# Optimization experiments

Measured on AMD Instinct MI355X. Metric: run time of the kernel, lower is better.

The kernel has to match this reference:

```python
import jax, jax.numpy as jnp
import numpy as np

N_HEADS = 32
N_KV = 8
GROUPS = 4
D_HEAD = 64
ROPE_BASE = 10000.0


def _rope_tables(seq_len):
    # inv_freq over even dims, emb = [freqs, freqs] along last axis (torch cat([outer]*2))
    inv_freq = 1.0 / (ROPE_BASE ** (jnp.arange(0, D_HEAD, 2, dtype=jnp.float32) / D_HEAD))
    t = jnp.arange(seq_len, dtype=jnp.float32)
    freqs = jnp.outer(t, inv_freq)                      # [S, D_HEAD/2]
    emb = jnp.concatenate([freqs, freqs], axis=-1)      # [S, D_HEAD]
    return jnp.cos(emb), jnp.sin(emb)


def _rotate_half(x):
    h = x.shape[-1] // 2
    return jnp.concatenate([-x[..., h:], x[..., :h]], axis=-1)


def setup_inputs() -> dict:
    key = jax.random.key(0)
    ks = jax.random.split(key, 5)
    B, S, D = 4, 2048, 2048
    s = 0.02
    return {
        "x": jax.random.normal(ks[0], (B, S, D), dtype=jnp.float32),
        "Wq": jax.random.normal(ks[1], (D, D), dtype=jnp.float32) * s,
        "Wk": jax.random.normal(ks[2], (N_KV * D_HEAD, D), dtype=jnp.float32) * s,
        "Wv": jax.random.normal(ks[3], (N_KV * D_HEAD, D), dtype=jnp.float32) * s,
        "Wo": jax.random.normal(ks[4], (D, D), dtype=jnp.float32) * s,
        "temperature": jnp.float32(1.0),
    }


def reference(x, Wq, Wk, Wv, Wo, temperature):
    B, S, D = x.shape
    # QKV projections (torch Linear: x @ W.T)
    Q = jnp.einsum('bsd,ed->bse', x, Wq).reshape(B, S, N_HEADS, D_HEAD).transpose(0, 2, 1, 3)
    K = jnp.einsum('bsd,ed->bse', x, Wk).reshape(B, S, N_KV, D_HEAD).transpose(0, 2, 1, 3)
    V = jnp.einsum('bsd,ed->bse', x, Wv).reshape(B, S, N_KV, D_HEAD).transpose(0, 2, 1, 3)

    # RoPE (offset=0, no past_kv)
    cos, sin = _rope_tables(S)          # [S, D_HEAD]
    cos = cos[None, None]
    sin = sin[None, None]
    Q = Q * cos + _rotate_half(Q) * sin
    K = K * cos + _rotate_half(K) * sin

    kv_cache = (K, V)  # pre-expansion cache, as in original

    # GQA expand: each kv head repeated GROUPS times along head axis
    Ke = jnp.repeat(K, GROUPS, axis=1)  # [B, N_HEADS, S, D_HEAD]
    Ve = jnp.repeat(V, GROUPS, axis=1)

    # scale uses .item() in torch -> constant w.r.t. autograd
    scale = (D_HEAD ** -0.5) / jnp.maximum(jnp.abs(temperature), 1e-6)
    scale = jax.lax.stop_gradient(scale)

    scores = jnp.einsum('bhqd,bhkd->bhqk', Q, Ke) * scale
    causal = jnp.tril(jnp.ones((S, S), dtype=bool))
    scores = jnp.where(causal[None, None], scores, jnp.finfo(scores.dtype).min)
    attn = jax.nn.softmax(scores, axis=-1)
    out = jnp.einsum('bhqk,bhkd->bhqd', attn, Ve)       # [B, H, S, D_HEAD]

    out = out.transpose(0, 2, 1, 3).reshape(B, S, D)
    y = jnp.einsum('bsd,ed->bse', out, Wo)
    return (y, kv_cache[0], kv_cache[1])
```

## Files before the change

### kernel.cpp

```cpp
#include <hip/hip_runtime.h>

#define S_LEN  2048
#define DMODEL 2048
#define NH     32
#define NKV    8
#define DH     64

typedef _Float16 h8   __attribute__((ext_vector_type(8)));
typedef _Float16 h4   __attribute__((ext_vector_type(4)));
typedef float    f32x4 __attribute__((ext_vector_type(4)));

__device__ __forceinline__ void load_lds16(const _Float16* g, _Float16* l) {
  typedef const __attribute__((address_space(1))) unsigned int* gp_t;
  typedef __attribute__((address_space(3))) unsigned int* lp_t;
  __builtin_amdgcn_global_load_lds((gp_t)g, (lp_t)l, 16, 0, 0);
}

#define N8_X  2097152
#define N8_WQ 524288
#define N8_WK 131072
#define N8_WV 131072
#define N8_WO 524288
#define N8_ALL (N8_X + N8_WQ + N8_WK + N8_WV + N8_WO)
__global__ void cvt_all(const float* __restrict__ x, const float* __restrict__ wq,
                        const float* __restrict__ wk, const float* __restrict__ wv,
                        const float* __restrict__ wo, _Float16* __restrict__ dst) {
  int stride = gridDim.x * blockDim.x;
  for (int i = blockIdx.x * blockDim.x + threadIdx.x; i < N8_ALL; i += stride) {
    const float* s;
    int off;
    if (i < N8_X) { s = x; off = i; }
    else if (i < N8_X + N8_WQ) { s = wq; off = i - N8_X; }
    else if (i < N8_X + N8_WQ + N8_WK) { s = wk; off = i - (N8_X + N8_WQ); }
    else if (i < N8_X + N8_WQ + N8_WK + N8_WV) { s = wv; off = i - (N8_X + N8_WQ + N8_WK); }
    else { s = wo; off = i - (N8_X + N8_WQ + N8_WK + N8_WV); }
    float4 a = ((const float4*)s)[2 * off];
    float4 b = ((const float4*)s)[2 * off + 1];
    h8 v = {(_Float16)a.x, (_Float16)a.y, (_Float16)a.z, (_Float16)a.w,
            (_Float16)b.x, (_Float16)b.y, (_Float16)b.z, (_Float16)b.w};
    ((h8*)dst)[i] = v;
  }
}

__global__ void rope_table_k(float2* __restrict__ tab) {
  int i = blockIdx.x * blockDim.x + threadIdx.x;
  int s = i >> 5, d = i & 31;
  float invf = (float)exp2(-(double)d * 0.4152410118609203);
  float angf = (float)s * invf;
  double a = (double)angf;
  const double twopi = 6.283185307179586476925287;
  a -= floor(a / twopi) * twopi;
  tab[i] = make_float2((float)cos(a), (float)sin(a));
}

template <int MODE>
__global__ __launch_bounds__(512, 2) void gemm256(
    const _Float16* __restrict__ A, const _Float16* __restrict__ Bm,
    _Float16* __restrict__ qH, _Float16* __restrict__ kH, float* __restrict__ kF,
    _Float16* __restrict__ vH, float* __restrict__ vF, float* __restrict__ yF,
    const float2* __restrict__ rtab, const float* __restrict__ tptr) {
  __shared__ __align__(16) _Float16 lA[2][256 * 64];
  __shared__ __align__(16) _Float16 lB[2][128 * 64];
  const int Kd = 2048;
  int t = threadIdx.x;
  int w = t >> 6, lane = t & 63;
  int n0 = blockIdx.x * 128, m0 = blockIdx.y * 256;
  int wr = w >> 1, wc = w & 1;
  int lq = lane & 15, hi = lane >> 4;

  int swz = ((lane & 7) ^ (lane >> 3)) * 8;
  const _Float16* pA = A + (size_t)(m0 + w * 32 + (lane >> 3)) * Kd + swz;
  const _Float16* pB = Bm + (size_t)(n0 + w * 16 + (lane >> 3)) * Kd + swz;
  int dA = (w * 32) * 64;
  int dB = (w * 16) * 64;

  f32x4 z4 = {0.f, 0.f, 0.f, 0.f};
  f32x4 acc[4][4];
#pragma unroll
  for (int i = 0; i < 4; i++)
#pragma unroll
    for (int j = 0; j < 4; j++) acc[i][j] = z4;

#pragma unroll
  for (int i = 0; i < 2; i++)
    load_lds16(pB + (size_t)(i * 8) * Kd, &lB[0][dB + i * 8 * 64]);
#pragma unroll
  for (int i = 0; i < 4; i++)
    load_lds16(pA + (size_t)(i * 8) * Kd, &lA[0][dA + i * 8 * 64]);

  const int NT = Kd / 64;
  for (int tt = 0; tt < NT; tt++) {
    int cur = tt & 1, nxt = cur ^ 1;

    asm volatile("s_waitcnt vmcnt(4)" ::: "memory");
    __builtin_amdgcn_s_barrier();

    if (tt + 1 < NT) {
      int k0n = (tt + 1) * 64;
#pragma unroll
      for (int i = 0; i < 2; i++)
        load_lds16(pB + (size_t)(i * 8) * Kd + k0n, &lB[nxt][dB + i * 8 * 64]);
#pragma unroll
      for (int i = 0; i < 4; i++)
        load_lds16(pA + (size_t)(i * 8) * Kd + k0n, &lA[nxt][dA + i * 8 * 64]);
    }

    h8 bf[4][2];
#pragma unroll
    for (int j = 0; j < 4; j++)
#pragma unroll
      for (int s = 0; s < 2; s++)
        bf[j][s] = *(const h8*)&lB[cur][(wc * 64 + j * 16 + lq) * 64 + (((s * 4 + hi) ^ (lq & 7)) * 8)];

    if (tt + 1 < NT) {
      asm volatile("s_waitcnt vmcnt(6)" ::: "memory");
    } else {
      asm volatile("s_waitcnt vmcnt(0)" ::: "memory");
    }
    __builtin_amdgcn_s_barrier();

#pragma unroll
    for (int p = 0; p < 4; p++) {
      h8 af[2];
#pragma unroll
      for (int s = 0; s < 2; s++)
        af[s] = *(const h8*)&lA[cur][(wr * 64 + p * 16 + lq) * 64 + (((s * 4 + hi) ^ (lq & 7)) * 8)];
      __builtin_amdgcn_s_setprio(1);
#pragma unroll
      for (int s = 0; s < 2; s++)
#pragma unroll
        for (int j = 0; j < 4; j++)
          acc[p][j] = __builtin_amdgcn_mfma_f32_16x16x32_f16(af[s], bf[j][s], acc[p][j], 0, 0, 0);
      __builtin_amdgcn_s_setprio(0);
    }
  }

  if (MODE == 3) {
#pragma unroll
    for (int ci = 0; ci < 4; ci++) {
      int col = n0 + wc * 64 + ci * 16 + lq;
#pragma unroll
      for (int i = 0; i < 4; i++)
#pragma unroll
        for (int r = 0; r < 4; r++) {
          int m = m0 + wr * 64 + i * 16 + hi * 4 + r;
          yF[(size_t)m * DMODEL + col] = acc[i][ci][r];
        }
    }
  } else {
    int base64 = n0 + wc * 64;
    if (base64 < 2048) {
      float qsc = 0.125f / fmaxf(fabsf(tptr[0]), 1e-6f) * 1.4426950408889634f;
      int head = base64 >> 6;
#pragma unroll
      for (int ci = 0; ci < 2; ci++) {
        int dlo = ci * 16 + lq;
#pragma unroll
        for (int i = 0; i < 4; i++)
#pragma unroll
          for (int r = 0; r < 4; r++) {
            int m = m0 + wr * 64 + i * 16 + hi * 4 + r;
            int b = m >> 11, s = m & 2047;
            float2 cs = rtab[s * 32 + dlo];
            float lo = acc[i][ci][r], hv = acc[i][ci + 2][r];
            float olo = (lo * cs.x - hv * cs.y) * qsc;
            float ohi = (hv * cs.x + lo * cs.y) * qsc;
            size_t base = ((size_t)(b * NH + head) * S_LEN + s) * DH;
            qH[base + dlo] = (_Float16)olo;
            qH[base + dlo + 32] = (_Float16)ohi;
          }
      }
    } else if (base64 < 2560) {
      int head = (base64 - 2048) >> 6;
#pragma unroll
      for (int ci = 0; ci < 2; ci++) {
        int dlo = ci * 16 + lq;
#pragma unroll
        for (int i = 0; i < 4; i++)
#pragma unroll
          for (int r = 0; r < 4; r++) {
            int m = m0 + wr * 64 + i * 16 + hi * 4 + r;
            int b = m >> 11, s = m & 2047;
            float2 cs = rtab[s * 32 + dlo];
            float lo = acc[i][ci][r], hv = acc[i][ci + 2][r];
            float olo = lo * cs.x - hv * cs.y;
            float ohi = hv * cs.x + lo * cs.y;
            size_t bb = ((size_t)(b * NKV + head) * S_LEN + s) * DH;
            kH[bb + dlo] = (_Float16)olo;
            kH[bb + dlo + 32] = (_Float16)ohi;
            kF[bb + dlo] = olo;
            kF[bb + dlo + 32] = ohi;
          }
      }
    } else {
      int head = (base64 - 2560) >> 6;
#pragma unroll
      for (int ci = 0; ci < 4; ci++) {
        int d = ci * 16 + lq;
#pragma unroll
        for (int i = 0; i < 4; i++)
#pragma unroll
          for (int r = 0; r < 4; r++) {
            int m = m0 + wr * 64 + i * 16 + hi * 4 + r;
            int b = m >> 11, s = m & 2047;
            float v = acc[i][ci][r];
            vH[((size_t)(b * NKV + head) * DH + d) * S_LEN + s] = (_Float16)v;
            vF[((size_t)(b * NKV + head) * S_LEN + s) * DH + d] = v;
          }
      }
    }
  }
}

__global__ __launch_bounds__(256, 3) void attn_fwd(
    const _Float16* __restrict__ Q, const _Float16* __restrict__ K,
    const _Float16* __restrict__ Vt, _Float16* __restrict__ AO) {
  __shared__ __align__(16) _Float16 lP[4][32 * 72];
  __shared__ __align__(16) _Float16 lK[2][64 * 64];
  __shared__ __align__(16) _Float16 lV[2][64 * 64];
  int t = threadIdx.x, w = t >> 6, lane = t & 63;
  int lq = lane & 15, hi = lane >> 4;

  int bh = blockIdx.x * 16 + (blockIdx.y & 15);
  int qb = 15 - (blockIdx.y >> 4);
  int b = bh >> 5, h = bh & 31, g = h >> 2;

  const _Float16* Qp = Q + ((size_t)(b * NH + h) * S_LEN) * DH;
  const _Float16* Kp = K + ((size_t)(b * NKV + g) * S_LEN) * DH;
  const _Float16* Vp = Vt + ((size_t)(b * NKV + g) * DH) * S_LEN;

  f32x4 z4 = {0.f, 0.f, 0.f, 0.f};
  int q0 = qb * 128 + w * 32;

  int swz = ((lane & 7) ^ (lane >> 3)) * 8;
  size_t sko0 = (size_t)(w * 16 + (lane >> 3)) * DH + (size_t)swz;
  size_t svo0 = (size_t)(w * 16 + (lane >> 3)) * S_LEN + (size_t)swz;

  h8 qf[2][2];
#pragma unroll
  for (int cf = 0; cf < 2; cf++)
#pragma unroll
    for (int dc = 0; dc < 2; dc++)
      qf[cf][dc] = *(const h8*)&Qp[(size_t)(q0 + lq + 16 * cf) * DH + dc * 32 + hi * 8];

  f32x4 ot[4][2];
#pragma unroll
  for (int rf = 0; rf < 4; rf++)
#pragma unroll
    for (int cf = 0; cf < 2; cf++) ot[rf][cf] = z4;
  float mrun[2] = {-3e38f, -3e38f};
  float lrun[2] = {0.f, 0.f};

  int NT = 2 * qb + 2;

  load_lds16(Kp + sko0, &lK[0][(w * 16) * 64]);
  load_lds16(Kp + sko0 + (size_t)8 * DH, &lK[0][(w * 16 + 8) * 64]);
  load_lds16(Vp + svo0, &lV[0][(w * 16) * 64]);
  load_lds16(Vp + svo0 + (size_t)8 * S_LEN, &lV[0][(w * 16 + 8) * 64]);

  for (int tk = 0; tk < NT; tk++) {
    int kv0 = tk * 64;

    asm volatile("s_waitcnt vmcnt(0)" ::: "memory");
    __builtin_amdgcn_s_barrier();

    if (tk + 1 < NT) {
      _Float16* nK = &lK[(tk + 1) & 1][0];
      _Float16* nV = &lV[(tk + 1) & 1][0];
      size_t kvn = (size_t)(kv0 + 64);
      load_lds16(Kp + kvn * DH + sko0, nK + (w * 16) * 64);
      load_lds16(Kp + kvn * DH + sko0 + (size_t)8 * DH, nK + (w * 16 + 8) * 64);
      load_lds16(Vp + svo0 + kvn, nV + (w * 16) * 64);
      load_lds16(Vp + svo0 + kvn + (size_t)8 * S_LEN, nV + (w * 16 + 8) * 64);
    }

    f32x4 sc[4][2];
#pragma unroll
    for (int rf = 0; rf < 4; rf++)
#pragma unroll
      for (int cf = 0; cf < 2; cf++) sc[rf][cf] = z4;
    {
      const _Float16* kb = &lK[tk & 1][0];
#pragma unroll
      for (int dc = 0; dc < 2; dc++) {
        h8 kf[4];
#pragma unroll
        for (int rf = 0; rf < 4; rf++)
          kf[rf] = *(const h8*)&kb[(rf * 16 + lq) * 64 + (((dc * 4 + hi) ^ (lq & 7)) * 8)];
#pragma unroll
        for (int rf = 0; rf < 4; rf++)
#pragma unroll
          for (int cf = 0; cf < 2; cf++)
            sc[rf][cf] = __builtin_amdgcn_mfma_f32_16x16x32_f16(kf[rf], qf[cf][dc], sc[rf][cf], 0, 0, 0);
      }
    }

    if (kv0 + 63 > q0) {
#pragma unroll
      for (int rf = 0; rf < 4; rf++)
#pragma unroll
        for (int cf = 0; cf < 2; cf++)
#pragma unroll
          for (int r = 0; r < 4; r++) {
            int kv = kv0 + rf * 16 + hi * 4 + r;
            int q = q0 + lq + 16 * cf;
            if (kv > q) sc[rf][cf][r] = -1e30f;
          }
    }

    float mt[2];
#pragma unroll
    for (int cf = 0; cf < 2; cf++) {
      float m2 = -3e38f;
#pragma unroll
      for (int rf = 0; rf < 4; rf++)
#pragma unroll
        for (int r = 0; r < 4; r++) m2 = fmaxf(m2, sc[rf][cf][r]);
      m2 = fmaxf(m2, __shfl_xor(m2, 16));
      m2 = fmaxf(m2, __shfl_xor(m2, 32));
      mt[cf] = m2;
    }

    bool need = !__all((mt[0] - mrun[0] <= 8.f) && (mt[1] - mrun[1] <= 8.f));
    if (need) {
#pragma unroll
      for (int cf = 0; cf < 2; cf++) {
        float mnew = fmaxf(mrun[cf], mt[cf]);
        float al = __builtin_amdgcn_exp2f(mrun[cf] - mnew);
        mrun[cf] = mnew;
        lrun[cf] *= al;
#pragma unroll
        for (int rf = 0; rf < 4; rf++)
#pragma unroll
          for (int r = 0; r < 4; r++) ot[rf][cf][r] *= al;
      }
    }

    float ls[2] = {0.f, 0.f};
#pragma unroll
    for (int rf = 0; rf < 4; rf++)
#pragma unroll
      for (int cf = 0; cf < 2; cf++)
#pragma unroll
        for (int r = 0; r < 4; r++) {
          float p = __builtin_amdgcn_exp2f(sc[rf][cf][r] - mrun[cf]);
          sc[rf][cf][r] = p;
          ls[cf] += p;
        }
#pragma unroll
    for (int cf = 0; cf < 2; cf++) {
      float s2 = ls[cf];
      s2 += __shfl_xor(s2, 16);
      s2 += __shfl_xor(s2, 32);
      lrun[cf] += s2;
    }

#pragma unroll
    for (int rf = 0; rf < 4; rf++)
#pragma unroll
      for (int cf = 0; cf < 2; cf++) {
        h4 p4;
#pragma unroll
        for (int r = 0; r < 4; r++) p4[r] = (_Float16)sc[rf][cf][r];
        *(h4*)&lP[w][(lq + 16 * cf) * 72 + rf * 16 + hi * 4] = p4;
      }
    asm volatile("s_waitcnt lgkmcnt(0)" ::: "memory");
    __builtin_amdgcn_sched_barrier(0);

    {
      const _Float16* vb = &lV[tk & 1][0];
#pragma unroll
      for (int kvc = 0; kvc < 2; kvc++) {
        h8 vf[4];
#pragma unroll
        for (int rf = 0; rf < 4; rf++)
          vf[rf] = *(const h8*)&vb[(rf * 16 + lq) * 64 + (((kvc * 4 + hi) ^ (lq & 7)) * 8)];
        h8 pb[2];
#pragma unroll
        for (int cf = 0; cf < 2; cf++)
          pb[cf] = *(const h8*)&lP[w][(lq + 16 * cf) * 72 + kvc * 32 + hi * 8];
#pragma unroll
        for (int rf = 0; rf < 4; rf++)
#pragma unroll
          for (int cf = 0; cf < 2; cf++)
            ot[rf][cf] = __builtin_amdgcn_mfma_f32_16x16x32_f16(vf[rf], pb[cf], ot[rf][cf], 0, 0, 0);
      }
    }
  }

#pragma unroll
  for (int cf = 0; cf < 2; cf++) {
    float inv = 1.0f / lrun[cf];
    size_t row = (size_t)b * S_LEN + q0 + lq + 16 * cf;
#pragma unroll
    for (int rf = 0; rf < 4; rf++) {
      h4 o;
#pragma unroll
      for (int r = 0; r < 4; r++) o[r] = (_Float16)(ot[rf][cf][r] * inv);
      *(h4*)&AO[row * DMODEL + h * DH + rf * 16 + hi * 4] = o;
    }
  }
}

extern "C" void kernel_launch(void* const* d_in, const int* in_sizes, int n_in,
                              void* d_out, int out_size, void* d_ws, size_t ws_size,
                              hipStream_t stream) {
  const float* x  = (const float*)d_in[0];
  const float* Wq = (const float*)d_in[1];
  const float* Wk = (const float*)d_in[2];
  const float* Wv = (const float*)d_in[3];
  const float* Wo = (const float*)d_in[4];
  const float* tp = (const float*)d_in[5];

  float* y  = (float*)d_out;
  float* Ko = y + (size_t)16777216;
  float* Vo = Ko + (size_t)4194304;

  _Float16* xh  = (_Float16*)d_ws;
  _Float16* wqh = xh + 16777216;
  _Float16* wkh = wqh + 4194304;
  _Float16* wvh = wkh + 1048576;
  _Float16* woh = wvh + 1048576;
  _Float16* Kh  = woh + 4194304;
  _Float16* Vth = Kh + 4194304;
  float2*   rtab = (float2*)(Vth + 4194304);
  _Float16* AOh = xh;
  _Float16* Qh  = (_Float16*)d_out;
  (void)wkh; (void)wvh;

  cvt_all<<<2048, 256, 0, stream>>>(x, Wq, Wk, Wv, Wo, xh);
  rope_table_k<<<256, 256, 0, stream>>>(rtab);

  gemm256<1><<<dim3(24, 32), 512, 0, stream>>>(xh, wqh, Qh, Kh, Ko, Vth, Vo, nullptr, rtab, tp);
  attn_fwd<<<dim3(8, 256), 256, 0, stream>>>(Qh, Kh, Vth, AOh);
  gemm256<3><<<dim3(16, 32), 512, 0, stream>>>(AOh, woh, nullptr, nullptr, nullptr, nullptr, nullptr, y, rtab, tp);
}
```

Before: 389.9 us.

## Split GEMM into QKV and output kernels with XCD-aware block remap and 256x256 tiles

```diff
diff --git a/kernel.cpp b/kernel.cpp
--- a/kernel.cpp
+++ b/kernel.cpp
@@ -53,18 +53,19 @@
   tab[i] = make_float2((float)cos(a), (float)sin(a));
 }
 
-template <int MODE>
-__global__ __launch_bounds__(512, 2) void gemm256(
+__global__ __launch_bounds__(512, 2) void gemm_qkv(
     const _Float16* __restrict__ A, const _Float16* __restrict__ Bm,
     _Float16* __restrict__ qH, _Float16* __restrict__ kH, float* __restrict__ kF,
-    _Float16* __restrict__ vH, float* __restrict__ vF, float* __restrict__ yF,
+    _Float16* __restrict__ vH, float* __restrict__ vF,
     const float2* __restrict__ rtab, const float* __restrict__ tptr) {
   __shared__ __align__(16) _Float16 lA[2][256 * 64];
   __shared__ __align__(16) _Float16 lB[2][128 * 64];
   const int Kd = 2048;
   int t = threadIdx.x;
   int w = t >> 6, lane = t & 63;
-  int n0 = blockIdx.x * 128, m0 = blockIdx.y * 256;
+  int bid = blockIdx.x;
+  int sid = (bid & 7) * 96 + (bid >> 3);
+  int n0 = (sid % 24) * 128, m0 = (sid / 24) * 256;
   int wr = w >> 1, wc = w & 1;
   int lq = lane & 15, hi = lane >> 4;
 
@@ -135,80 +136,163 @@
     }
   }
 
-  if (MODE == 3) {
-#pragma unroll
-    for (int ci = 0; ci < 4; ci++) {
-      int col = n0 + wc * 64 + ci * 16 + lq;
+  int base64 = n0 + wc * 64;
+  if (base64 < 2048) {
+    float qsc = 0.125f / fmaxf(fabsf(tptr[0]), 1e-6f) * 1.4426950408889634f;
+    int head = base64 >> 6;
+#pragma unroll
+    for (int ci = 0; ci < 2; ci++) {
+      int dlo = ci * 16 + lq;
 #pragma unroll
       for (int i = 0; i < 4; i++)
 #pragma unroll
         for (int r = 0; r < 4; r++) {
           int m = m0 + wr * 64 + i * 16 + hi * 4 + r;
-          yF[(size_t)m * DMODEL + col] = acc[i][ci][r];
+          int b = m >> 11, s = m & 2047;
+          float2 cs = rtab[s * 32 + dlo];
+          float lo = acc[i][ci][r], hv = acc[i][ci + 2][r];
+          float olo = (lo * cs.x - hv * cs.y) * qsc;
+          float ohi = (hv * cs.x + lo * cs.y) * qsc;
+          size_t base = ((size_t)(b * NH + head) * S_LEN + s) * DH;
+          qH[base + dlo] = (_Float16)olo;
+          qH[base + dlo + 32] = (_Float16)ohi;
         }
     }
+  } else if (base64 < 2560) {
+    int head = (base64 - 2048) >> 6;
+#pragma unroll
+    for (int ci = 0; ci < 2; ci++) {
+      int dlo = ci * 16 + lq;
+#pragma unroll
+      for (int i = 0; i < 4; i++)
+#pragma unroll
+        for (int r = 0; r < 4; r++) {
+          int m = m0 + wr * 64 + i * 16 + hi * 4 + r;
+          int b = m >> 11, s = m & 2047;
+          float2 cs = rtab[s * 32 + dlo];
+          float lo = acc[i][ci][r], hv = acc[i][ci + 2][r];
+          float olo = lo * cs.x - hv * cs.y;
+          float ohi = hv * cs.x + lo * cs.y;
+          size_t bb = ((size_t)(b * NKV + head) * S_LEN + s) * DH;
+          kH[bb + dlo] = (_Float16)olo;
+          kH[bb + dlo + 32] = (_Float16)ohi;
+          kF[bb + dlo] = olo;
+          kF[bb + dlo + 32] = ohi;
+        }
+    }
   } else {
-    int base64 = n0 + wc * 64;
-    if (base64 < 2048) {
-      float qsc = 0.125f / fmaxf(fabsf(tptr[0]), 1e-6f) * 1.4426950408889634f;
-      int head = base64 >> 6;
-#pragma unroll
-      for (int ci = 0; ci < 2; ci++) {
-        int dlo = ci * 16 + lq;
-#pragma unroll
-        for (int i = 0; i < 4; i++)
-#pragma unroll
-          for (int r = 0; r < 4; r++) {
-            int m = m0 + wr * 64 + i * 16 + hi * 4 + r;
-            int b = m >> 11, s = m & 2047;
-            float2 cs = rtab[s * 32 + dlo];
-            float lo = acc[i][ci][r], hv = acc[i][ci + 2][r];
-            float olo = (lo * cs.x - hv * cs.y) * qsc;
-            float ohi = (hv * cs.x + lo * cs.y) * qsc;
-            size_t base = ((size_t)(b * NH + head) * S_LEN + s) * DH;
-            qH[base + dlo] = (_Float16)olo;
-            qH[base + dlo + 32] = (_Float16)ohi;
-          }
+    int head = (base64 - 2560) >> 6;
+#pragma unroll
+    for (int ci = 0; ci < 4; ci++) {
+      int d = ci * 16 + lq;
+#pragma unroll
+      for (int i = 0; i < 4; i++)
+#pragma unroll
+        for (int r = 0; r < 4; r++) {
+          int m = m0 + wr * 64 + i * 16 + hi * 4 + r;
+          int b = m >> 11, s = m & 2047;
+          float v = acc[i][ci][r];
+          vH[((size_t)(b * NKV + head) * DH + d) * S_LEN + s] = (_Float16)v;
+          vF[((size_t)(b * NKV + head) * S_LEN + s) * DH + d] = v;
+        }
+    }
+  }
+}
+
+__global__ __launch_bounds__(512, 2) void gemm_out(
+    const _Float16* __restrict__ A, const _Float16* __restrict__ Bm,
+    float* __restrict__ yF) {
+  __shared__ __align__(16) _Float16 lA[2][256 * 64];
+  __shared__ __align__(16) _Float16 lB[2][256 * 64];
+  const int Kd = 2048;
+  int t = threadIdx.x;
+  int w = t >> 6, lane = t & 63;
+  int bid = blockIdx.x;
+  int sid = (bid & 7) * 32 + (bid >> 3);
+  int n0 = (sid & 7) * 256, m0 = (sid >> 3) * 256;
+  int wr = w >> 2, wc = w & 3;
+  int lq = lane & 15, hi = lane >> 4;
+
+  int swz = ((lane & 7) ^ (lane >> 3)) * 8;
+  const _Float16* pA = A + (size_t)(m0 + w * 32 + (lane >> 3)) * Kd + swz;
+  const _Float16* pB = Bm + (size_t)(n0 + w * 32 + (lane >> 3)) * Kd + swz;
+  int dRow = (w * 32) * 64;
+
+  f32x4 z4 = {0.f, 0.f, 0.f, 0.f};
+  f32x4 acc[8][4];
+#pragma unroll
+  for (int i = 0; i < 8; i++)
+#pragma unroll
+    for (int j = 0; j < 4; j++) acc[i][j] = z4;
+
+#pragma unroll
+  for (int i = 0; i < 4; i++)
+    load_lds16(pB + (size_t)(i * 8) * Kd, &lB[0][dRow + i * 8 * 64]);
+#pragma unroll
+  for (int i = 0; i < 4; i++)
+    load_lds16(pA + (size_t)(i * 8) * Kd, &lA[0][dRow + i * 8 * 64]);
+
+  const int NT = Kd / 64;
+  for (int tt = 0; tt < NT; tt++) {
+    int cur = tt & 1, nxt = cur ^ 1;
+
+    asm volatile("s_waitcnt vmcnt(4)" ::: "memory");
+    __builtin_amdgcn_s_barrier();
+
+    if (tt + 1 < NT) {
+      int k0n = (tt + 1) * 64;
+#pragma unroll
+      for (int i = 0; i < 4; i++)
+        load_lds16(pB + (size_t)(i * 8) * Kd + k0n, &lB[nxt][dRow + i * 8 * 64]);
+#pragma unroll
+      for (int i = 0; i < 4; i++)
+        load_lds16(pA + (size_t)(i * 8) * Kd + k0n, &lA[nxt][dRow + i * 8 * 64]);
+    }
+
+    h8 bf[4][2];
+#pragma unroll
+    for (int j = 0; j < 4; j++)
+#pragma unroll
+      for (int s = 0; s < 2; s++)
+        bf[j][s] = *(const h8*)&lB[cur][(wc * 64 + j * 16 + lq) * 64 + (((s * 4 + hi) ^ (lq & 7)) * 8)];
+
+    if (tt + 1 < NT) {
+      asm volatile("s_waitcnt vmcnt(8)" ::: "memory");
+    } else {
+      asm volatile("s_waitcnt vmcnt(0)" ::: "memory");
+    }
+    __builtin_amdgcn_s_barrier();
+
+#pragma unroll
+    for (int p = 0; p < 4; p++) {
+      h8 af[2][2];
+#pragma unroll
+      for (int di = 0; di < 2; di++)
+#pragma unroll
+        for (int s = 0; s < 2; s++)
+          af[di][s] = *(const h8*)&lA[cur][(wr * 128 + (p * 2 + di) * 16 + lq) * 64 + (((s * 4 + hi) ^ (lq & 7)) * 8)];
+      __builtin_amdgcn_s_setprio(1);
+#pragma unroll
+      for (int s = 0; s < 2; s++)
+#pragma unroll
+        for (int di = 0; di < 2; di++)
+#pragma unroll
+          for (int j = 0; j < 4; j++)
+            acc[p * 2 + di][j] = __builtin_amdgcn_mfma_f32_16x16x32_f16(af[di][s], bf[j][s], acc[p * 2 + di][j], 0, 0, 0);
+      __builtin_amdgcn_s_setprio(0);
+    }
+  }
+
+#pragma unroll
+  for (int ci = 0; ci < 4; ci++) {
+    int col = n0 + wc * 64 + ci * 16 + lq;
+#pragma unroll
+    for (int i = 0; i < 8; i++)
+#pragma unroll
+      for (int r = 0; r < 4; r++) {
+        int m = m0 + wr * 128 + i * 16 + hi * 4 + r;
+        yF[(size_t)m * DMODEL + col] = acc[i][ci][r];
       }
-    } else if (base64 < 2560) {
-      int head = (base64 - 2048) >> 6;
-#pragma unroll
-      for (int ci = 0; ci < 2; ci++) {
-        int dlo = ci * 16 + lq;
-#pragma unroll
-        for (int i = 0; i < 4; i++)
-#pragma unroll
-          for (int r = 0; r < 4; r++) {
-            int m = m0 + wr * 64 + i * 16 + hi * 4 + r;
-            int b = m >> 11, s = m & 2047;
-            float2 cs = rtab[s * 32 + dlo];
-            float lo = acc[i][ci][r], hv = acc[i][ci + 2][r];
-            float olo = lo * cs.x - hv * cs.y;
-            float ohi = hv * cs.x + lo * cs.y;
-            size_t bb = ((size_t)(b * NKV + head) * S_LEN + s) * DH;
-            kH[bb + dlo] = (_Float16)olo;
-            kH[bb + dlo + 32] = (_Float16)ohi;
-            kF[bb + dlo] = olo;
-            kF[bb + dlo + 32] = ohi;
-          }
-      }
-    } else {
-      int head = (base64 - 2560) >> 6;
-#pragma unroll
-      for (int ci = 0; ci < 4; ci++) {
-        int d = ci * 16 + lq;
-#pragma unroll
-        for (int i = 0; i < 4; i++)
-#pragma unroll
-          for (int r = 0; r < 4; r++) {
-            int m = m0 + wr * 64 + i * 16 + hi * 4 + r;
-            int b = m >> 11, s = m & 2047;
-            float v = acc[i][ci][r];
-            vH[((size_t)(b * NKV + head) * DH + d) * S_LEN + s] = (_Float16)v;
-            vF[((size_t)(b * NKV + head) * S_LEN + s) * DH + d] = v;
-          }
-      }
-    }
   }
 }
 
@@ -431,7 +515,7 @@
   cvt_all<<<2048, 256, 0, stream>>>(x, Wq, Wk, Wv, Wo, xh);
   rope_table_k<<<256, 256, 0, stream>>>(rtab);
 
-  gemm256<1><<<dim3(24, 32), 512, 0, stream>>>(xh, wqh, Qh, Kh, Ko, Vth, Vo, nullptr, rtab, tp);
+  gemm_qkv<<<768, 512, 0, stream>>>(xh, wqh, Qh, Kh, Ko, Vth, Vo, rtab, tp);
   attn_fwd<<<dim3(8, 256), 256, 0, stream>>>(Qh, Kh, Vth, AOh);
-  gemm256<3><<<dim3(16, 32), 512, 0, stream>>>(AOh, woh, nullptr, nullptr, nullptr, nullptr, nullptr, y, rtab, tp);
-}
+  gemm_out<<<256, 512, 0, stream>>>(AOh, woh, y);
+}
```

Measured after the change: 371.4 us. 1.05x faster.
